# Kernel tuning notes

Hardware: AMD Instinct MI355X
Metric: run time of the kernel (lower is better)

Reference implementation:

```python
import jax, jax.numpy as jnp
import numpy as np

N = 50000          # num_nodes
IN_F = 256
OUT_F = 256
R = 2
LEV = 2
L = R * LEV        # number of sparse framelet operators
NNZ = 800000       # nonzeros per operator (avg degree 16)
THRESHOLD = 1e-4


def _spmm(rows, cols, vals, x, n):
    # y = D @ x for COO sparse D of shape [n, n]
    return jax.ops.segment_sum(vals[:, None] * x[cols], rows, num_segments=n)


def setup_inputs() -> dict:
    key = jax.random.key(0)
    ks = jax.random.split(key, 7)
    x = jax.random.normal(ks[0], (N, IN_F), dtype=jnp.float32)
    # xavier-uniform-ish weight
    bound = np.sqrt(6.0 / (IN_F + OUT_F))
    weight = jax.random.uniform(ks[1], (IN_F, OUT_F), dtype=jnp.float32,
                                minval=-bound, maxval=bound)
    # filter init uniform(0.9, 1.1) as in reset_parameters
    filt = jax.random.uniform(ks[2], (R * LEV * N, 1), dtype=jnp.float32,
                              minval=0.9, maxval=1.1)
    bias = jax.random.normal(ks[3], (OUT_F,), dtype=jnp.float32) * 0.02
    # COO sparse framelet operators, scaled small to keep the chained
    # products numerically tame
    d_vals = jax.random.normal(ks[4], (L, NNZ), dtype=jnp.float32) * 0.05
    d_rows = jax.random.randint(ks[5], (L, NNZ), 0, N, dtype=jnp.int32)
    d_cols = jax.random.randint(ks[6], (L, NNZ), 0, N, dtype=jnp.int32)
    return {"x": x, "weight": weight, "filt": filt, "bias": bias,
            "d_vals": d_vals, "d_rows": d_rows, "d_cols": d_cols}


def reference(x, weight, filt, bias, d_vals, d_rows, d_cols):
    h = x @ weight                                   # [N, OUT_F]
    # fast tight-frame decomposition: chained SpMMs
    for i in range(L):
        h = _spmm(d_rows[i], d_cols[i], d_vals[i], h, N)
    # soft shrinkage
    h = jnp.sign(h) * jax.nn.relu(jnp.abs(h) - THRESHOLD)
    # learned per-row filter (first N rows of the [r*Lev*N, 1] filter)
    h = h * filt[: h.shape[0]]
    # reconstruction: operators Lev-1 .. L-1
    for i in range(LEV - 1, L):
        h = _spmm(d_rows[i], d_cols[i], d_vals[i], h, N)
    return h + bias
```

## Files before the change

kernel.cpp:

```cpp
#include <hip/hip_runtime.h>
#include <hip/hip_bf16.h>

#define N_NODES 50000
#define NNZ 800000
#define F 256
#define L_OPS 4
#define ELL_C 64
#define RTILES 3125
#define NBK 98
#define CHUNKS 391

typedef unsigned int uint;
typedef unsigned short u16;
typedef unsigned char u8;
typedef unsigned long long u64;
typedef __attribute__((ext_vector_type(8))) short bf16x8;
typedef __attribute__((ext_vector_type(4))) float f32x4;
typedef __attribute__((ext_vector_type(2))) float f32x2;

#if defined(__has_builtin)
#if __has_builtin(__builtin_amdgcn_cvt_pk_f32_fp8) && \
    __has_builtin(__builtin_amdgcn_cvt_pk_fp8_f32)
#define HAS_FP8_CVT 1
#endif
#endif

__device__ inline u16 f2bf(float f) {
  return __bfloat16_as_ushort(__float2bfloat16(f));
}
__device__ inline float shrinkf(float f) {
  float t = fabsf(f) - 1e-4f;
  t = t > 0.f ? t : 0.f;
  return copysignf(t, f);
}

__device__ inline uint fp8_enc1(float f) {
#ifdef HAS_FP8_CVT
  return (uint)__builtin_amdgcn_cvt_pk_fp8_f32(f, 0.f, 0, false) & 0xFFu;
#else
  float y = f * 0x1.0p-120f;
  uint b = __float_as_uint(y);
  uint s = (b >> 24) & 0x80u;
  b &= 0x7FFFFFFFu;
  uint r = b + 0x7FFFFu + ((b >> 20) & 1u);
  return s | ((r >> 20) & 0x7Fu);
#endif
}
__device__ inline uint fp8_enc4(float a, float b, float c, float d) {
#ifdef HAS_FP8_CVT
  uint w = (uint)__builtin_amdgcn_cvt_pk_fp8_f32(a, b, 0, false);
  w = (uint)__builtin_amdgcn_cvt_pk_fp8_f32(c, d, w, true);
  return w;
#else
  return fp8_enc1(a) | (fp8_enc1(b) << 8) | (fp8_enc1(c) << 16) |
         (fp8_enc1(d) << 24);
#endif
}
__device__ inline float fp8_dec1(uint b) {
  uint u = ((b & 0x80u) << 24) | ((b & 0x7Fu) << 20);
  return __uint_as_float(u) * 0x1.0p+120f;
}

__global__ __launch_bounds__(256) void wprep_k(const float* __restrict__ W,
                                               u16* __restrict__ Wb) {
  int T = blockIdx.x * 256 + threadIdx.x;
  if (T >= 16 * 8 * 64) return;
  int lane = T & 63;
  int ks = (T >> 6) & 7;
  int ct = T >> 9;
  int k0 = ks * 32 + (lane >> 4) * 8;
  int n = ct * 16 + (lane & 15);
  u16* o = Wb + (size_t)T * 8;
#pragma unroll
  for (int j = 0; j < 8; ++j) o[j] = f2bf(W[(size_t)(k0 + j) * F + n]);
}

__global__ __launch_bounds__(256) void gemm_mfma(const float* __restrict__ X,
                                                 const u16* __restrict__ Wb,
                                                 u8* __restrict__ H) {
  const int w = threadIdx.x >> 6, lane = threadIdx.x & 63;
  const int lr = lane & 15, kg = lane >> 4;
  const int ct0 = w * 4;

  bf16x8 b[4][8];
#pragma unroll
  for (int c = 0; c < 4; ++c)
#pragma unroll
    for (int ks = 0; ks < 8; ++ks)
      b[c][ks] = *(const bf16x8*)(Wb + ((size_t)((ct0 + c) * 8 + ks) * 64 + lane) * 8);

  for (int tile = blockIdx.x; tile < RTILES; tile += gridDim.x) {
    const int rb = tile * 16;
    const float* xp = X + (size_t)(rb + lr) * F + kg * 8;
    f32x4 acc[4];
#pragma unroll
    for (int c = 0; c < 4; ++c) acc[c] = (f32x4){0.f, 0.f, 0.f, 0.f};
#pragma unroll
    for (int ks = 0; ks < 8; ++ks) {
      float4 x0 = *(const float4*)(xp + ks * 32);
      float4 x1 = *(const float4*)(xp + ks * 32 + 4);
      bf16x8 a;
      a[0] = (short)f2bf(x0.x); a[1] = (short)f2bf(x0.y);
      a[2] = (short)f2bf(x0.z); a[3] = (short)f2bf(x0.w);
      a[4] = (short)f2bf(x1.x); a[5] = (short)f2bf(x1.y);
      a[6] = (short)f2bf(x1.z); a[7] = (short)f2bf(x1.w);
#pragma unroll
      for (int c = 0; c < 4; ++c)
        acc[c] = __builtin_amdgcn_mfma_f32_16x16x32_bf16(a, b[c][ks], acc[c], 0, 0, 0);
    }
    const int r0 = rb + kg * 4;
#pragma unroll
    for (int c = 0; c < 4; ++c)
#pragma unroll
      for (int reg = 0; reg < 4; ++reg)
        H[(size_t)(r0 + reg) * F + (ct0 + c) * 16 + lr] =
            (u8)fp8_enc1(acc[c][reg] * 16.f);
  }
}

__global__ __launch_bounds__(256) void b1_hist(const int* __restrict__ rows,
                                               int* __restrict__ hoff) {
  const int op = blockIdx.y, c = blockIdx.x;
  __shared__ int h[NBK];
  for (int t = threadIdx.x; t < NBK; t += 256) h[t] = 0;
  __syncthreads();
  const int* rop = rows + (size_t)op * NNZ;
  const int base = c * 2048 + threadIdx.x;
#pragma unroll
  for (int it = 0; it < 8; ++it) {
    int i = base + it * 256;
    if (i < NNZ) atomicAdd(&h[rop[i] >> 9], 1);
  }
  __syncthreads();
  for (int t = threadIdx.x; t < NBK; t += 256)
    hoff[((size_t)op * CHUNKS + c) * NBK + t] = h[t];
}

__global__ __launch_bounds__(512) void b2a_scan(int* __restrict__ hoff,
                                                int* __restrict__ tot) {
  const int op = blockIdx.y, b = blockIdx.x, t = threadIdx.x;
  __shared__ int sh[512];
  int v = (t < CHUNKS) ? hoff[((size_t)op * CHUNKS + t) * NBK + b] : 0;
  sh[t] = v;
  __syncthreads();
#pragma unroll
  for (int off = 1; off < 512; off <<= 1) {
    int tmp = (t >= off) ? sh[t - off] : 0;
    __syncthreads();
    sh[t] += tmp;
    __syncthreads();
  }
  if (t < CHUNKS) hoff[((size_t)op * CHUNKS + t) * NBK + b] = sh[t] - v;
  if (t == 511) tot[op * NBK + b] = sh[511];
}

__global__ __launch_bounds__(128) void b2b_base(const int* __restrict__ tot,
                                                int* __restrict__ bs) {
  const int op = blockIdx.x, t = threadIdx.x;
  __shared__ int sh[128];
  int v = (t < NBK) ? tot[op * NBK + t] : 0;
  sh[t] = v;
  __syncthreads();
#pragma unroll
  for (int off = 1; off < 128; off <<= 1) {
    int tmp = (t >= off) ? sh[t - off] : 0;
    __syncthreads();
    sh[t] += tmp;
    __syncthreads();
  }
  if (t < NBK) bs[op * NBK + t] = sh[t] - v;
}

__global__ __launch_bounds__(256) void b3_scatter(const int* __restrict__ rows,
                                                  const int* __restrict__ cols,
                                                  const float* __restrict__ vals,
                                                  const int* __restrict__ hoff,
                                                  const int* __restrict__ bs,
                                                  u64* __restrict__ part) {
  const int op = blockIdx.y, c = blockIdx.x;
  __shared__ int cur[NBK];
  for (int t = threadIdx.x; t < NBK; t += 256)
    cur[t] = op * NNZ + bs[op * NBK + t] + hoff[((size_t)op * CHUNKS + c) * NBK + t];
  __syncthreads();
  const int* rop = rows + (size_t)op * NNZ;
  const int* cop = cols + (size_t)op * NNZ;
  const float* vop = vals + (size_t)op * NNZ;
  const int base = c * 2048 + threadIdx.x;
#pragma unroll
  for (int it = 0; it < 8; ++it) {
    int i = base + it * 256;
    if (i < NNZ) {
      int r = rop[i];
      int p = atomicAdd(&cur[r >> 9], 1);
      uint cv = ((uint)f2bf(vop[i]) << 16) | (uint)cop[i];
      part[p] = ((u64)cv << 32) | (uint)(r & 511);
    }
  }
}

__global__ __launch_bounds__(256) void b4_build(const u64* __restrict__ part,
                                                const int* __restrict__ bs,
                                                const int* __restrict__ tot,
                                                uint* __restrict__ ell,
                                                int* __restrict__ cnt) {
  const int op = blockIdx.y, b = blockIdx.x;
  __shared__ int c[512];
  for (int t = threadIdx.x; t < 512; t += 256) c[t] = 0;
  __syncthreads();
  const int s = bs[op * NBK + b], n = tot[op * NBK + b];
  const u64* seg = part + (size_t)op * NNZ + s;
  uint* ellb = ell + (size_t)op * N_NODES * ELL_C + (size_t)b * 512 * ELL_C;
  for (int i = threadIdx.x; i < n; i += 256) {
    u64 w = seg[i];
    int rl = (int)(w & 0xFFFFu);
    int p = atomicAdd(&c[rl], 1);
    if (p < ELL_C) ellb[rl * ELL_C + p] = (uint)(w >> 32);
  }
  __syncthreads();
  const int nrow = min(512, N_NODES - b * 512);
  int* cb = cnt + (size_t)op * N_NODES + b * 512;
  for (int t = threadIdx.x; t < nrow; t += 256) cb[t] = c[t];
}

#define PROC(cv)                                                          \
  {                                                                       \
    uint c_ = (cv) & 0xFFFFu;                                             \
    float v_ = __uint_as_float((cv) & 0xFFFF0000u);                       \
    uint g = *(const uint*)(hinL + (size_t)c_ * F);                       \
    f32x2 glo, ghi;                                                       \
    DEC4(g, glo, ghi);                                                    \
    a0 = fmaf(v_, glo[0], a0);                                            \
    a1 = fmaf(v_, glo[1], a1);                                            \
    a2 = fmaf(v_, ghi[0], a2);                                            \
    a3 = fmaf(v_, ghi[1], a3);                                            \
  }

#ifdef HAS_FP8_CVT
#define DEC4(g, lo, hi)                                                   \
  lo = __builtin_amdgcn_cvt_pk_f32_fp8((g), false);                       \
  hi = __builtin_amdgcn_cvt_pk_f32_fp8((g), true);
#else
#define DEC4(g, lo, hi)                                                   \
  lo[0] = fp8_dec1((g) & 0xFFu); lo[1] = fp8_dec1(((g) >> 8) & 0xFFu);    \
  hi[0] = fp8_dec1(((g) >> 16) & 0xFFu); hi[1] = fp8_dec1((g) >> 24);
#endif

template <int MODE>
__global__ __launch_bounds__(256) void spmm_k(const int* __restrict__ cnt,
                                              const uint* __restrict__ ell,
                                              const u8* __restrict__ hin,
                                              void* __restrict__ out,
                                              const float* __restrict__ filt,
                                              const float* __restrict__ bias,
                                              float m1, float m2) {
  const int lane = threadIdx.x & 63;
  const int r = blockIdx.x * 4 + (threadIdx.x >> 6);
  if (r >= N_NODES) return;
  int e = cnt[r];
  e = e < ELL_C ? e : ELL_C;
  const uint* __restrict__ row = ell + (size_t)r * ELL_C;
  const u8* __restrict__ hinL = hin + lane * 4;
  float a0 = 0.f, a1 = 0.f, a2 = 0.f, a3 = 0.f;
  int j = 0;
  for (; j + 8 <= e; j += 8) {
    uint4 q0 = *(const uint4*)(row + j);
    uint4 q1 = *(const uint4*)(row + j + 4);
    PROC(q0.x); PROC(q0.y); PROC(q0.z); PROC(q0.w);
    PROC(q1.x); PROC(q1.y); PROC(q1.z); PROC(q1.w);
  }
  for (; j + 4 <= e; j += 4) {
    uint4 q = *(const uint4*)(row + j);
    PROC(q.x); PROC(q.y); PROC(q.z); PROC(q.w);
  }
  for (; j < e; ++j) {
    uint cv = row[j];
    PROC(cv);
  }
  if (MODE == 0) {
    uint w = fp8_enc4(a0 * m1, a1 * m1, a2 * m1, a3 * m1);
    *(uint*)((u8*)out + (size_t)r * F + lane * 4) = w;
  } else if (MODE == 1) {
    float fl = filt[r] * m2;
    uint w = fp8_enc4(shrinkf(a0 * m1) * fl, shrinkf(a1 * m1) * fl,
                      shrinkf(a2 * m1) * fl, shrinkf(a3 * m1) * fl);
    *(uint*)((u8*)out + (size_t)r * F + lane * 4) = w;
  } else {
    float4 b = *(const float4*)(bias + lane * 4);
    float4 o;
    o.x = fmaf(a0, m1, b.x); o.y = fmaf(a1, m1, b.y);
    o.z = fmaf(a2, m1, b.z); o.w = fmaf(a3, m1, b.w);
    *(float4*)((float*)out + (size_t)r * F + lane * 4) = o;
  }
}

extern "C" void kernel_launch(void* const* d_in, const int* in_sizes, int n_in,
                              void* d_out, int out_size, void* d_ws, size_t ws_size,
                              hipStream_t stream) {
  const float* X = (const float*)d_in[0];
  const float* W = (const float*)d_in[1];
  const float* filt = (const float*)d_in[2];
  const float* bias = (const float*)d_in[3];
  const float* dvals = (const float*)d_in[4];
  const int* drows = (const int*)d_in[5];
  const int* dcols = (const int*)d_in[6];

  char* p = (char*)d_ws;
  auto alloc = [&](size_t bytes) {
    char* q = p;
    p += (bytes + 255) & ~(size_t)255;
    return q;
  };
  u8* hA = (u8*)alloc((size_t)N_NODES * F);
  u8* hB = (u8*)alloc((size_t)N_NODES * F);
  u16* Wb = (u16*)alloc((size_t)F * F * 2);
  int* cnt = (int*)alloc((size_t)L_OPS * N_NODES * 4);
  uint* ell = (uint*)alloc((size_t)L_OPS * N_NODES * ELL_C * 4);
  u64* part = (u64*)alloc((size_t)L_OPS * NNZ * 8);
  int* hoff = (int*)alloc((size_t)L_OPS * CHUNKS * NBK * 4);
  int* tot = (int*)alloc((size_t)L_OPS * NBK * 4);
  int* bs = (int*)alloc((size_t)L_OPS * NBK * 4);

  b1_hist<<<dim3(CHUNKS, L_OPS), 256, 0, stream>>>(drows, hoff);
  b2a_scan<<<dim3(NBK, L_OPS), 512, 0, stream>>>(hoff, tot);
  b2b_base<<<L_OPS, 128, 0, stream>>>(tot, bs);
  b3_scatter<<<dim3(CHUNKS, L_OPS), 256, 0, stream>>>(drows, dcols, dvals,
                                                      hoff, bs, part);
  b4_build<<<dim3(NBK, L_OPS), 256, 0, stream>>>(part, bs, tot, ell, cnt);

  wprep_k<<<64, 256, 0, stream>>>(W, Wb);
  gemm_mfma<<<1024, 256, 0, stream>>>(X, Wb, hA);

  auto sp = [&](int op, const u8* in, void* out, int mode, float m1, float m2) {
    const int* co = cnt + (size_t)op * N_NODES;
    const uint* eo = ell + (size_t)op * N_NODES * ELL_C;
    dim3 g((N_NODES + 3) / 4);
    if (mode == 0)
      spmm_k<0><<<g, 256, 0, stream>>>(co, eo, in, out, filt, bias, m1, m2);
    else if (mode == 1)
      spmm_k<1><<<g, 256, 0, stream>>>(co, eo, in, out, filt, bias, m1, m2);
    else
      spmm_k<2><<<g, 256, 0, stream>>>(co, eo, in, out, filt, bias, m1, m2);
  };

  sp(0, hA, hB, 0, 4.f, 0.f);
  sp(1, hB, hA, 0, 4.f, 0.f);
  sp(2, hA, hB, 0, 4.f, 0.f);
  sp(3, hB, hA, 1, 0x1.0p-10f, 0x1.0p+13f);
  sp(1, hA, hB, 0, 4.f, 0.f);
  sp(2, hB, hA, 0, 4.f, 0.f);
  sp(3, hA, d_out, 2, 0x1.0p-17f, 0.f);
}
```

Before: 324.1 us.

## Slice feature matrix into 32-column panels and stage COO scatter in LDS

The intermediate fp8 feature matrix is stored as eight 32-byte column slices, one contiguous [N,32] panel each. Each SpMM block now handles one slice for 32 rows, so the gathered working set per slice is about 1.6 MB and should stay cache-resident instead of spanning all 256 columns. The bucket scatter now sorts each 4096-entry chunk in shared memory before writing, turning random global writes into mostly contiguous runs. The cost is that each ELL row index list is re-read eight times, one per slice, and each gather moves only 4 bytes per lane. The scatter also gains a larger LDS footprint and an extra scan.

```diff
diff --git a/kernel.cpp b/kernel.cpp
--- a/kernel.cpp
+++ b/kernel.cpp
@@ -8,7 +8,9 @@
 #define ELL_C 64
 #define RTILES 3125
 #define NBK 98
-#define CHUNKS 391
+#define CHUNK 4096
+#define CHUNKS 196
+#define N32 (N_NODES * 32)
 
 typedef unsigned int uint;
 typedef unsigned short u16;
@@ -110,11 +112,14 @@
     }
     const int r0 = rb + kg * 4;
 #pragma unroll
-    for (int c = 0; c < 4; ++c)
+    for (int c = 0; c < 4; ++c) {
+      const int col = (ct0 + c) * 16 + lr;
+      const int slice = col >> 5, within = col & 31;
 #pragma unroll
       for (int reg = 0; reg < 4; ++reg)
-        H[(size_t)(r0 + reg) * F + (ct0 + c) * 16 + lr] =
+        H[(size_t)slice * N32 + (size_t)(r0 + reg) * 32 + within] =
             (u8)fp8_enc1(acc[c][reg] * 16.f);
+    }
   }
 }
 
@@ -125,9 +130,9 @@
   for (int t = threadIdx.x; t < NBK; t += 256) h[t] = 0;
   __syncthreads();
   const int* rop = rows + (size_t)op * NNZ;
-  const int base = c * 2048 + threadIdx.x;
-#pragma unroll
-  for (int it = 0; it < 8; ++it) {
+  const int base = c * CHUNK + threadIdx.x;
+#pragma unroll
+  for (int it = 0; it < 16; ++it) {
     int i = base + it * 256;
     if (i < NNZ) atomicAdd(&h[rop[i] >> 9], 1);
   }
@@ -178,23 +183,60 @@
                                                   const int* __restrict__ bs,
                                                   u64* __restrict__ part) {
   const int op = blockIdx.y, c = blockIdx.x;
+  __shared__ int hist[NBK];
+  __shared__ int lstart[NBK];
+  __shared__ int gbase[NBK];
   __shared__ int cur[NBK];
-  for (int t = threadIdx.x; t < NBK; t += 256)
-    cur[t] = op * NNZ + bs[op * NBK + t] + hoff[((size_t)op * CHUNKS + c) * NBK + t];
+  __shared__ int sh[256];
+  __shared__ u64 stage[CHUNK];
+  const int t = threadIdx.x;
+  for (int k = t; k < NBK; k += 256) hist[k] = 0;
   __syncthreads();
   const int* rop = rows + (size_t)op * NNZ;
   const int* cop = cols + (size_t)op * NNZ;
   const float* vop = vals + (size_t)op * NNZ;
-  const int base = c * 2048 + threadIdx.x;
-#pragma unroll
-  for (int it = 0; it < 8; ++it) {
-    int i = base + it * 256;
+  const int n0 = c * CHUNK;
+  const int nthis = min(CHUNK, NNZ - n0);
+#pragma unroll
+  for (int it = 0; it < 16; ++it) {
+    int i = n0 + it * 256 + t;
+    if (i < NNZ) atomicAdd(&hist[rop[i] >> 9], 1);
+  }
+  __syncthreads();
+  int v = (t < NBK) ? hist[t] : 0;
+  sh[t] = v;
+  __syncthreads();
+#pragma unroll
+  for (int off = 1; off < 256; off <<= 1) {
+    int tmp = (t >= off) ? sh[t - off] : 0;
+    __syncthreads();
+    sh[t] += tmp;
+    __syncthreads();
+  }
+  if (t < NBK) {
+    int ex = sh[t] - v;
+    lstart[t] = ex;
+    cur[t] = ex;
+    gbase[t] = op * NNZ + bs[op * NBK + t] +
+               hoff[((size_t)op * CHUNKS + c) * NBK + t];
+  }
+  __syncthreads();
+#pragma unroll
+  for (int it = 0; it < 16; ++it) {
+    int i = n0 + it * 256 + t;
     if (i < NNZ) {
       int r = rop[i];
-      int p = atomicAdd(&cur[r >> 9], 1);
+      int b = r >> 9;
+      int p = atomicAdd(&cur[b], 1);
       uint cv = ((uint)f2bf(vop[i]) << 16) | (uint)cop[i];
-      part[p] = ((u64)cv << 32) | (uint)(r & 511);
+      stage[p] = ((u64)cv << 32) | (uint)(b << 9) | (uint)(r & 511);
     }
+  }
+  __syncthreads();
+  for (int q = t; q < nthis; q += 256) {
+    u64 w = stage[q];
+    int b = (int)((w >> 9) & 127u);
+    part[(size_t)gbase[b] + (q - lstart[b])] = w;
   }
 }
 
@@ -212,7 +254,7 @@
   uint* ellb = ell + (size_t)op * N_NODES * ELL_C + (size_t)b * 512 * ELL_C;
   for (int i = threadIdx.x; i < n; i += 256) {
     u64 w = seg[i];
-    int rl = (int)(w & 0xFFFFu);
+    int rl = (int)(w & 0x1FFu);
     int p = atomicAdd(&c[rl], 1);
     if (p < ELL_C) ellb[rl * ELL_C + p] = (uint)(w >> 32);
   }
@@ -221,19 +263,6 @@
   int* cb = cnt + (size_t)op * N_NODES + b * 512;
   for (int t = threadIdx.x; t < nrow; t += 256) cb[t] = c[t];
 }
-
-#define PROC(cv)                                                          \
-  {                                                                       \
-    uint c_ = (cv) & 0xFFFFu;                                             \
-    float v_ = __uint_as_float((cv) & 0xFFFF0000u);                       \
-    uint g = *(const uint*)(hinL + (size_t)c_ * F);                       \
-    f32x2 glo, ghi;                                                       \
-    DEC4(g, glo, ghi);                                                    \
-    a0 = fmaf(v_, glo[0], a0);                                            \
-    a1 = fmaf(v_, glo[1], a1);                                            \
-    a2 = fmaf(v_, ghi[0], a2);                                            \
-    a3 = fmaf(v_, ghi[1], a3);                                            \
-  }
 
 #ifdef HAS_FP8_CVT
 #define DEC4(g, lo, hi)                                                   \
@@ -245,6 +274,19 @@
   hi[0] = fp8_dec1(((g) >> 16) & 0xFFu); hi[1] = fp8_dec1((g) >> 24);
 #endif
 
+#define PROC(cv)                                                          \
+  {                                                                       \
+    uint c_ = (cv) & 0xFFFFu;                                             \
+    float v_ = __uint_as_float((cv) & 0xFFFF0000u);                       \
+    uint g = *(const uint*)(hs + (size_t)c_ * 32);                        \
+    f32x2 glo, ghi;                                                       \
+    DEC4(g, glo, ghi);                                                    \
+    a0 = fmaf(v_, glo[0], a0);                                            \
+    a1 = fmaf(v_, glo[1], a1);                                            \
+    a2 = fmaf(v_, ghi[0], a2);                                            \
+    a3 = fmaf(v_, ghi[1], a3);                                            \
+  }
+
 template <int MODE>
 __global__ __launch_bounds__(256) void spmm_k(const int* __restrict__ cnt,
                                               const uint* __restrict__ ell,
@@ -253,13 +295,16 @@
                                               const float* __restrict__ filt,
                                               const float* __restrict__ bias,
                                               float m1, float m2) {
+  const int slice = blockIdx.x & 7;
   const int lane = threadIdx.x & 63;
-  const int r = blockIdx.x * 4 + (threadIdx.x >> 6);
+  const int w = threadIdx.x >> 6;
+  const int r = (blockIdx.x >> 3) * 32 + w * 8 + (lane >> 3);
+  const int word = lane & 7;
   if (r >= N_NODES) return;
   int e = cnt[r];
   e = e < ELL_C ? e : ELL_C;
   const uint* __restrict__ row = ell + (size_t)r * ELL_C;
-  const u8* __restrict__ hinL = hin + lane * 4;
+  const u8* __restrict__ hs = hin + (size_t)slice * N32 + word * 4;
   float a0 = 0.f, a1 = 0.f, a2 = 0.f, a3 = 0.f;
   int j = 0;
   for (; j + 8 <= e; j += 8) {
@@ -277,19 +322,19 @@
     PROC(cv);
   }
   if (MODE == 0) {
-    uint w = fp8_enc4(a0 * m1, a1 * m1, a2 * m1, a3 * m1);
-    *(uint*)((u8*)out + (size_t)r * F + lane * 4) = w;
+    uint o = fp8_enc4(a0 * m1, a1 * m1, a2 * m1, a3 * m1);
+    *(uint*)((u8*)out + (size_t)slice * N32 + (size_t)r * 32 + word * 4) = o;
   } else if (MODE == 1) {
     float fl = filt[r] * m2;
-    uint w = fp8_enc4(shrinkf(a0 * m1) * fl, shrinkf(a1 * m1) * fl,
+    uint o = fp8_enc4(shrinkf(a0 * m1) * fl, shrinkf(a1 * m1) * fl,
                       shrinkf(a2 * m1) * fl, shrinkf(a3 * m1) * fl);
-    *(uint*)((u8*)out + (size_t)r * F + lane * 4) = w;
+    *(uint*)((u8*)out + (size_t)slice * N32 + (size_t)r * 32 + word * 4) = o;
   } else {
-    float4 b = *(const float4*)(bias + lane * 4);
+    float4 b = *(const float4*)(bias + slice * 32 + word * 4);
     float4 o;
     o.x = fmaf(a0, m1, b.x); o.y = fmaf(a1, m1, b.y);
     o.z = fmaf(a2, m1, b.z); o.w = fmaf(a3, m1, b.w);
-    *(float4*)((float*)out + (size_t)r * F + lane * 4) = o;
+    *(float4*)((float*)out + (size_t)r * F + slice * 32 + word * 4) = o;
   }
 }
 
@@ -333,7 +378,7 @@
   auto sp = [&](int op, const u8* in, void* out, int mode, float m1, float m2) {
     const int* co = cnt + (size_t)op * N_NODES;
     const uint* eo = ell + (size_t)op * N_NODES * ELL_C;
-    dim3 g((N_NODES + 3) / 4);
+    dim3 g(((N_NODES + 31) / 32) * 8);
     if (mode == 0)
       spmm_k<0><<<g, 256, 0, stream>>>(co, eo, in, out, filt, bias, m1, m2);
     else if (mode == 1)
```

After: 379.8 us. +17.2%, slower.
